# Optimization experiments

Hardware: AMD Instinct MI355X
Metric: run time of the kernel (lower is better)

Reference implementation:

```python
import jax, jax.numpy as jnp
import numpy as np

V_DECAY = float(np.exp(-1.0 / 100.0))   # voltage_tau = 100
S_DECAY = float(np.exp(-1.0 / 50.0))    # synapse_tau = 50
THRESH = 1.0                            # spiking_threshold

N_IN = 8192
N_OUT = 8192


def setup_inputs() -> dict:
    key = jax.random.key(0)
    k1, k2, k3, k4 = jax.random.split(key, 4)
    input_spikes = jax.random.uniform(k1, (N_IN,), dtype=jnp.float32)
    voltages = jax.random.normal(k2, (1, N_OUT), dtype=jnp.float32)
    synapses = jax.random.normal(k3, (N_IN, N_OUT), dtype=jnp.float32)
    weights = jax.random.normal(k4, (N_IN, N_OUT), dtype=jnp.float32)
    return {"input_spikes": input_spikes, "voltages": voltages,
            "synapses": synapses, "weights": weights}


def reference(input_spikes, voltages, synapses, weights):
    # voltages *= voltage_decay
    v = voltages * V_DECAY                              # [1, n_out]
    # output_spikes = voltages >= threshold (computed on decayed voltage)
    spikes = v >= THRESH                                # [1, n_out] bool
    # synapses *= synapse_decay; per-column loop == rank-1 broadcast add
    syn = synapses * S_DECAY + weights * input_spikes[:, None]  # [n_in, n_out]
    # voltages += synapses.sum(dim=0) - spikes * threshold
    v_new = v + syn.sum(axis=0) - spikes.astype(v.dtype) * THRESH  # [1, n_out]
    return spikes, v_new, syn
```

## Files before the change

kernel.cpp:

```cpp
#include <hip/hip_runtime.h>


#define V_DECAY 0.99004983374916811f
#define S_DECAY 0.98019867330675525f
#define THRESH  1.0f

constexpr int N_IN  = 8192;
constexpr int N_OUT = 8192;
constexpr int COLS_PER_BLOCK = 1024;
constexpr int COL_TILES = N_OUT / COLS_PER_BLOCK;

typedef float f32x4 __attribute__((ext_vector_type(4)));

__global__ __launch_bounds__(256) void lif_syn_kernel(
    const float* __restrict__ input_spikes,
    const float* __restrict__ synapses,
    const float* __restrict__ weights,
    float* __restrict__ syn_out,
    float* __restrict__ partials,
    int rowsPerChunk)
{
    const int ct   = blockIdx.x % COL_TILES;
    const int rc   = blockIdx.x / COL_TILES;
    const int col  = ct * COLS_PER_BLOCK + threadIdx.x * 4;
    const int row0 = rc * rowsPerChunk;

    f32x4 acc = (f32x4)(0.f);
    #pragma unroll 4
    for (int r = 0; r < rowsPerChunk; ++r) {
        const int row    = row0 + r;
        const size_t idx = (size_t)row * N_OUT + col;
        const f32x4 s4 = *reinterpret_cast<const f32x4*>(synapses + idx);
        const f32x4 w4 = *reinterpret_cast<const f32x4*>(weights  + idx);
        const float sp = input_spikes[row];
        const f32x4 o  = s4 * S_DECAY + w4 * sp;
        __builtin_nontemporal_store(o, reinterpret_cast<f32x4*>(syn_out + idx));
        acc += o;
    }
    __builtin_nontemporal_store(
        acc, reinterpret_cast<f32x4*>(partials + (size_t)rc * N_OUT + col));
}

__global__ __launch_bounds__(256) void lif_v_kernel(
    const float* __restrict__ voltages,
    const float* __restrict__ partials,
    float* __restrict__ out,
    int rowChunks)
{
    const int c = blockIdx.x * blockDim.x + threadIdx.x;
    const float v     = voltages[c] * V_DECAY;
    const float spike = (v >= THRESH) ? 1.0f : 0.0f;
    float sum = 0.f;
    #pragma unroll 4
    for (int rc = 0; rc < rowChunks; ++rc)
        sum += partials[(size_t)rc * N_OUT + c];
    out[c]          = spike;
    out[N_OUT + c]  = v + sum - spike * THRESH;
}

extern "C" void kernel_launch(void* const* d_in, const int* in_sizes, int n_in,
                              void* d_out, int out_size, void* d_ws, size_t ws_size,
                              hipStream_t stream) {
    const float* input_spikes = (const float*)d_in[0];
    const float* voltages     = (const float*)d_in[1];
    const float* synapses     = (const float*)d_in[2];
    const float* weights      = (const float*)d_in[3];

    float* out      = (float*)d_out;
    float* syn_out  = out + 2 * N_OUT;
    float* partials = (float*)d_ws;

    int rowChunks = 512;
    while (rowChunks > 1 &&
           (size_t)rowChunks * N_OUT * sizeof(float) > ws_size)
        rowChunks >>= 1;
    const int rowsPerChunk = N_IN / rowChunks;

    lif_syn_kernel<<<dim3(COL_TILES * rowChunks), dim3(256), 0, stream>>>(
        input_spikes, synapses, weights, syn_out, partials, rowsPerChunk);

    lif_v_kernel<<<dim3(N_OUT / 256), dim3(256), 0, stream>>>(
        voltages, partials, out, rowChunks);
}
```

Baseline: 206.4 us.

## Widen blocks to two column strips and cut row-chunk count for fewer partials

Each block now covers 2048 columns: every thread handles two float4 strips 1024 apart with separate accumulators, which doubles memory-level parallelism per thread. The row chunk count drops from 512 to 128, so the grid shrinks from 4096 to 512 blocks, each looping over 64 rows instead of 16, and the partials buffer and the final reduction pass get smaller. The output stores and the partials stores switch from nontemporal to ordinary stores, which may pollute the cache while streaming 256MB of output. The smaller grid risks lower occupancy across the CUs.

Measured after the change: 175.5 us. -14.9%, faster.

```diff
diff --git a/kernel.cpp b/kernel.cpp
--- a/kernel.cpp
+++ b/kernel.cpp
@@ -7,8 +7,8 @@
 
 constexpr int N_IN  = 8192;
 constexpr int N_OUT = 8192;
-constexpr int COLS_PER_BLOCK = 1024;
-constexpr int COL_TILES = N_OUT / COLS_PER_BLOCK;
+constexpr int COLSPLIT = 4;
+constexpr int COLS = N_OUT / COLSPLIT;
 
 typedef float f32x4 __attribute__((ext_vector_type(4)));
 
@@ -20,42 +20,49 @@
     float* __restrict__ partials,
     int rowsPerChunk)
 {
-    const int ct   = blockIdx.x % COL_TILES;
-    const int rc   = blockIdx.x / COL_TILES;
-    const int col  = ct * COLS_PER_BLOCK + threadIdx.x * 4;
+    const int ct   = blockIdx.x % COLSPLIT;
+    const int rc   = blockIdx.x / COLSPLIT;
+    const int c0   = ct * COLS + threadIdx.x * 4;
     const int row0 = rc * rowsPerChunk;
 
-    f32x4 acc = (f32x4)(0.f);
+    f32x4 acc0 = (f32x4)(0.f), acc1 = (f32x4)(0.f);
+
     #pragma unroll 4
     for (int r = 0; r < rowsPerChunk; ++r) {
         const int row    = row0 + r;
-        const size_t idx = (size_t)row * N_OUT + col;
-        const f32x4 s4 = *reinterpret_cast<const f32x4*>(synapses + idx);
-        const f32x4 w4 = *reinterpret_cast<const f32x4*>(weights  + idx);
-        const float sp = input_spikes[row];
-        const f32x4 o  = s4 * S_DECAY + w4 * sp;
-        __builtin_nontemporal_store(o, reinterpret_cast<f32x4*>(syn_out + idx));
-        acc += o;
+        const float sp   = input_spikes[row];
+        const size_t b   = (size_t)row * N_OUT + c0;
+        const f32x4 s0 = *(const f32x4*)(synapses + b);
+        const f32x4 s1 = *(const f32x4*)(synapses + b + 1024);
+        const f32x4 w0 = *(const f32x4*)(weights  + b);
+        const f32x4 w1 = *(const f32x4*)(weights  + b + 1024);
+        const f32x4 o0 = s0 * S_DECAY + w0 * sp;
+        const f32x4 o1 = s1 * S_DECAY + w1 * sp;
+        *(f32x4*)(syn_out + b)        = o0;
+        *(f32x4*)(syn_out + b + 1024) = o1;
+        acc0 += o0; acc1 += o1;
     }
-    __builtin_nontemporal_store(
-        acc, reinterpret_cast<f32x4*>(partials + (size_t)rc * N_OUT + col));
+
+    const size_t pbase = (size_t)rc * N_OUT + c0;
+    *(f32x4*)(partials + pbase)        = acc0;
+    *(f32x4*)(partials + pbase + 1024) = acc1;
 }
 
 __global__ __launch_bounds__(256) void lif_v_kernel(
     const float* __restrict__ voltages,
     const float* __restrict__ partials,
     float* __restrict__ out,
-    int rowChunks)
+    int nChunks)
 {
     const int c = blockIdx.x * blockDim.x + threadIdx.x;
     const float v     = voltages[c] * V_DECAY;
     const float spike = (v >= THRESH) ? 1.0f : 0.0f;
     float sum = 0.f;
-    #pragma unroll 4
-    for (int rc = 0; rc < rowChunks; ++rc)
-        sum += partials[(size_t)rc * N_OUT + c];
-    out[c]          = spike;
-    out[N_OUT + c]  = v + sum - spike * THRESH;
+    #pragma unroll 8
+    for (int g = 0; g < nChunks; ++g)
+        sum += partials[(size_t)g * N_OUT + c];
+    out[c]         = spike;
+    out[N_OUT + c] = v + sum - spike * THRESH;
 }
 
 extern "C" void kernel_launch(void* const* d_in, const int* in_sizes, int n_in,
@@ -70,15 +77,14 @@
     float* syn_out  = out + 2 * N_OUT;
     float* partials = (float*)d_ws;
 
-    int rowChunks = 512;
-    while (rowChunks > 1 &&
-           (size_t)rowChunks * N_OUT * sizeof(float) > ws_size)
-        rowChunks >>= 1;
-    const int rowsPerChunk = N_IN / rowChunks;
+    int chunks = 128;
+    while (chunks > 1 && (size_t)chunks * N_OUT * sizeof(float) > ws_size)
+        chunks >>= 1;
+    const int rowsPerChunk = N_IN / chunks;
 
-    lif_syn_kernel<<<dim3(COL_TILES * rowChunks), dim3(256), 0, stream>>>(
+    lif_syn_kernel<<<dim3(COLSPLIT * chunks), dim3(256), 0, stream>>>(
         input_spikes, synapses, weights, syn_out, partials, rowsPerChunk);
 
     lif_v_kernel<<<dim3(N_OUT / 256), dim3(256), 0, stream>>>(
-        voltages, partials, out, rowChunks);
+        voltages, partials, out, chunks);
 }
```
